# Kernel tuning notes

Hardware: AMD Instinct MI355X
Metric: run time of the kernel (lower is better)

## Reference

```python
import jax, jax.numpy as jnp
import numpy as np

B, T, D, H, L, V = 2, 1024, 1024, 16, 4, 32000
HS = D // H  # head_size = 64


def setup_inputs() -> dict:
    key = jax.random.key(0)
    ks = jax.random.split(key, 15)
    s = 0.02
    return {
        "idx": jax.random.randint(ks[0], (B, T), 0, V, dtype=jnp.int32),
        "tok_emb": jax.random.normal(ks[1], (V, D), jnp.float32) * s,
        "pos_emb": jax.random.normal(ks[2], (T, D), jnp.float32) * s,
        "Wq": jax.random.normal(ks[3], (L, H, D, HS), jnp.float32) * s,
        "Wk": jax.random.normal(ks[4], (L, H, D, HS), jnp.float32) * s,
        "Wv": jax.random.normal(ks[5], (L, H, D, HS), jnp.float32) * s,
        "Wproj": jax.random.normal(ks[6], (L, D, D), jnp.float32) * s,
        "bproj": jnp.zeros((L, D), jnp.float32),
        "W1": jax.random.normal(ks[7], (L, D, 4 * D), jnp.float32) * s,
        "b1": jnp.zeros((L, 4 * D), jnp.float32),
        "W2": jax.random.normal(ks[8], (L, 4 * D, D), jnp.float32) * s,
        "b2": jnp.zeros((L, D), jnp.float32),
        "Wlm": jax.random.normal(ks[9], (D, V), jnp.float32) * s,
        "blm": jnp.zeros((V,), jnp.float32),
    }


def reference(idx, tok_emb, pos_emb, Wq, Wk, Wv, Wproj, bproj, W1, b1, W2, b2, Wlm, blm):
    Bn, Tn = idx.shape
    Dn = tok_emb.shape[1]
    x = tok_emb[idx] + pos_emb[jnp.arange(Tn)][None, :, :]  # (B,T,D)
    causal = jnp.tril(jnp.ones((Tn, Tn), dtype=bool))
    # NOTE: original scales by C**-0.5 where C = embedding_dim (not head_size)
    scale = Dn ** -0.5
    n_layers = Wq.shape[0]
    for l in range(n_layers):
        q = jnp.einsum('btd,hdk->bhtk', x, Wq[l])
        k = jnp.einsum('btd,hdk->bhtk', x, Wk[l])
        v = jnp.einsum('btd,hdk->bhtk', x, Wv[l])
        scores = jnp.einsum('bhtk,bhsk->bhts', q, k) * scale
        scores = jnp.where(causal[None, None, :, :], scores, -jnp.inf)
        probs = jax.nn.softmax(scores, axis=-1)
        attn = jnp.einsum('bhts,bhsk->bhtk', probs, v)
        # concat heads in head order -> (B,T,H*HS)
        attn = attn.transpose(0, 2, 1, 3).reshape(Bn, Tn, Dn)
        x = x + attn @ Wproj[l] + bproj[l]
        h = jax.nn.relu(x @ W1[l] + b1[l])
        x = x + h @ W2[l] + b2[l]
    return x @ Wlm + blm  # (B,T,V) logits
```

## Files before the change

### kernel.cpp

```cpp
#include <hip/hip_runtime.h>
#include <stdint.h>

#define DEVI static __device__ __forceinline__

typedef __attribute__((ext_vector_type(8))) _Float16  f16x8;
typedef __attribute__((ext_vector_type(8))) uint16_t  u16x8;
typedef __attribute__((ext_vector_type(4))) uint16_t  u16x4;
typedef __attribute__((ext_vector_type(4))) float     f32x4;

DEVI uint16_t f2h(float f){ return __builtin_bit_cast(uint16_t, (_Float16)f); }

DEVI void gload_lds16(const void* g, void* l){
  __builtin_amdgcn_global_load_lds((__attribute__((address_space(1))) void*)g,
                                   (__attribute__((address_space(3))) void*)l, 16, 0, 0);
}
DEVI f16x8 frag_ld(const void* base, int byteoff){
  const u16x8* p = (const u16x8*)((const char*)base + byteoff);
  return __builtin_bit_cast(f16x8, *p);
}

__global__ __launch_bounds__(256) void transpose_f32_f16(
    const float* __restrict__ in, uint16_t* __restrict__ out,
    int ld_in, int ld_out,
    long long in_z, long long out_zA, long long out_zB, int zdiv)
{
  __shared__ float tile[64][65];
  const int r0 = blockIdx.x * 64, c0 = blockIdx.y * 64;
  const int z  = blockIdx.z;
  const float* inp = in + (long long)z * in_z;
  uint16_t* outp = out + (long long)(z / zdiv) * out_zA + (long long)(z % zdiv) * out_zB;
  const int r16 = threadIdx.x >> 4, c4 = (threadIdx.x & 15) * 4;
  #pragma unroll
  for (int i = 0; i < 4; i++){
    int r = i * 16 + r16;
    const float4 v = *(const float4*)(inp + (long long)(r0 + r) * ld_in + (c0 + c4));
    tile[r][c4] = v.x; tile[r][c4 + 1] = v.y; tile[r][c4 + 2] = v.z; tile[r][c4 + 3] = v.w;
  }
  __syncthreads();
  const int rp = (threadIdx.x & 31) * 2;
  const int cy = threadIdx.x >> 5;
  #pragma unroll
  for (int i = 0; i < 8; i++){
    int c = i * 8 + cy;
    uint32_t v = (uint32_t)f2h(tile[rp][c]) | ((uint32_t)f2h(tile[rp + 1][c]) << 16);
    *(uint32_t*)(outp + (long long)(c0 + c) * ld_out + (r0 + rp)) = v;
  }
}

__global__ __launch_bounds__(256) void embed_kernel(
    const int* __restrict__ idx, const float* __restrict__ tok,
    const float* __restrict__ pos, float* __restrict__ xf, uint16_t* __restrict__ xb)
{
  const int t = blockIdx.x;
  const int d = threadIdx.x * 4;
  const int token = idx[t];
  const int tp = t & 1023;
  const float4 tv = *(const float4*)(tok + (size_t)token * 1024 + d);
  const float4 pv = *(const float4*)(pos + (size_t)tp * 1024 + d);
  float4 s; s.x = tv.x + pv.x; s.y = tv.y + pv.y; s.z = tv.z + pv.z; s.w = tv.w + pv.w;
  *(float4*)(xf + (size_t)t * 1024 + d) = s;
  uint16_t* o = xb + (size_t)t * 1024 + d;
  o[0] = f2h(s.x); o[1] = f2h(s.y); o[2] = f2h(s.z); o[3] = f2h(s.w);
}

template<bool SPLITK, bool BIAS, bool RELU, bool RES, bool OUTF, bool OUTB, bool QSCALE>
__global__ __launch_bounds__(256, 3) void gemm_bt(
    const uint16_t* __restrict__ A, const uint16_t* __restrict__ Bt,
    const float* __restrict__ bias, const float* __restrict__ res,
    float* __restrict__ outf, uint16_t* __restrict__ outb,
    int M, int N, int K)
{
  __shared__ __align__(16) uint16_t As[128 * 64];
  __shared__ __align__(16) uint16_t Bs[128 * 64];
  const int tid = threadIdx.x, lane = tid & 63, wid = tid >> 6;

  const int Mt = M >> 7;
  int flat = blockIdx.x;
  int kidx = 0;
  if constexpr (SPLITK){ kidx = flat & 1; flat >>= 1; }
  const int total = SPLITK ? (gridDim.x >> 1) : gridDim.x;
  const int wg = (flat & 7) * (total >> 3) + (flat >> 3);
  const int bm = (wg % Mt) * 128, bn = (wg / Mt) * 128;
  int k0 = 0, k1 = K;
  if constexpr (SPLITK){ const int Kh = K >> 1; k0 = kidx * Kh; k1 = k0 + Kh; }
  float* outp = outf;
  if constexpr (SPLITK) outp = outf + (size_t)kidx * M * N;

  const uint16_t* gA[4]; const uint16_t* gB[4];
  #pragma unroll
  for (int i = 0; i < 4; i++){
    int c = i * 256 + tid;
    int row = c >> 3;
    int p = (c * 16) ^ ((row & 7) << 4);
    int off = (p >> 1) & 63;
    gA[i] = A  + (size_t)(bm + row) * K + off;
    gB[i] = Bt + (size_t)(bn + row) * K + off;
  }

  f32x4 acc[4][4];
  const f32x4 fz = {0.f, 0.f, 0.f, 0.f};
  #pragma unroll
  for (int a = 0; a < 4; a++)
    #pragma unroll
    for (int n = 0; n < 4; n++) acc[a][n] = fz;

  const int lrow = lane & 15, lk2 = (lane >> 4) * 16;
  const int wr = (wid >> 1) * 64, wc = (wid & 1) * 64;

  for (int kt = k0; kt < k1; kt += 64){
    #pragma unroll
    for (int i = 0; i < 4; i++)
      gload_lds16(gA[i] + kt, (char*)As + (i * 256 + wid * 64) * 16);
    #pragma unroll
    for (int i = 0; i < 4; i++)
      gload_lds16(gB[i] + kt, (char*)Bs + (i * 256 + wid * 64) * 16);
    __syncthreads();
    #pragma unroll
    for (int kk = 0; kk < 2; kk++){
      f16x8 af[4], bfv[4];
      #pragma unroll
      for (int mf = 0; mf < 4; mf++){
        int row = wr + mf * 16 + lrow;
        af[mf] = frag_ld(As, (row * 128 + kk * 64 + lk2) ^ ((row & 7) << 4));
      }
      #pragma unroll
      for (int nf = 0; nf < 4; nf++){
        int row = wc + nf * 16 + lrow;
        bfv[nf] = frag_ld(Bs, (row * 128 + kk * 64 + lk2) ^ ((row & 7) << 4));
      }
      #pragma unroll
      for (int mf = 0; mf < 4; mf++)
        #pragma unroll
        for (int nf = 0; nf < 4; nf++)
          acc[mf][nf] = __builtin_amdgcn_mfma_f32_16x16x32_f16(af[mf], bfv[nf], acc[mf][nf], 0, 0, 0);
    }
    __syncthreads();
  }

  #pragma unroll
  for (int mf = 0; mf < 4; mf++){
    const int row0 = bm + wr + mf * 16 + (lane >> 4) * 4;
    #pragma unroll
    for (int nf = 0; nf < 4; nf++){
      const int col = bn + wc + nf * 16 + (lane & 15);
      float bv = 0.f;
      if constexpr (BIAS) bv = bias[col];
      float qs = 1.0f;
      if constexpr (QSCALE) qs = (col < 1024) ? 0.03125f : 1.0f;
      #pragma unroll
      for (int j = 0; j < 4; j++){
        float v = acc[mf][nf][j] + bv;
        size_t oi = (size_t)(row0 + j) * N + col;
        if constexpr (RES)  v += res[oi];
        if constexpr (RELU) v = fmaxf(v, 0.f);
        if constexpr (OUTF) outp[oi] = v;
        if constexpr (OUTB) outb[oi] = f2h(v * qs);
      }
    }
  }
}

__global__ __launch_bounds__(256, 2) void gemm_lm(
    const uint16_t* __restrict__ A, const uint16_t* __restrict__ Bt,
    const float* __restrict__ bias, float* __restrict__ outf,
    int M, int N, int K)
{
  __shared__ __align__(16) uint16_t As[128 * 64];
  __shared__ __align__(16) uint16_t Bs[256 * 64];
  const int tid = threadIdx.x, lane = tid & 63, wid = tid >> 6;

  const int Mt = M >> 7;
  const int flat = blockIdx.x;
  const int wg = (flat & 7) * (gridDim.x >> 3) + (flat >> 3);
  const int bm = (wg % Mt) * 128, bn = (wg / Mt) * 256;

  const uint16_t* gA[4]; const uint16_t* gB[8];
  #pragma unroll
  for (int i = 0; i < 4; i++){
    int c = i * 256 + tid;
    int row = c >> 3;
    int p = (c * 16) ^ ((row & 7) << 4);
    int off = (p >> 1) & 63;
    gA[i] = A + (size_t)(bm + row) * K + off;
  }
  #pragma unroll
  for (int i = 0; i < 8; i++){
    int c = i * 256 + tid;
    int row = c >> 3;
    int p = (c * 16) ^ ((row & 7) << 4);
    int off = (p >> 1) & 63;
    gB[i] = Bt + (size_t)(bn + row) * K + off;
  }

  f32x4 acc[4][8];
  const f32x4 fz = {0.f, 0.f, 0.f, 0.f};
  #pragma unroll
  for (int a = 0; a < 4; a++)
    #pragma unroll
    for (int n = 0; n < 8; n++) acc[a][n] = fz;

  const int lrow = lane & 15, lk2 = (lane >> 4) * 16;
  const int wr = (wid >> 1) * 64, wc = (wid & 1) * 128;

  for (int kt = 0; kt < K; kt += 64){
    #pragma unroll
    for (int i = 0; i < 4; i++)
      gload_lds16(gA[i] + kt, (char*)As + (i * 256 + wid * 64) * 16);
    #pragma unroll
    for (int i = 0; i < 8; i++)
      gload_lds16(gB[i] + kt, (char*)Bs + (i * 256 + wid * 64) * 16);
    __syncthreads();
    #pragma unroll
    for (int kk = 0; kk < 2; kk++){
      f16x8 af[4], bfv[8];
      #pragma unroll
      for (int mf = 0; mf < 4; mf++){
        int row = wr + mf * 16 + lrow;
        af[mf] = frag_ld(As, (row * 128 + kk * 64 + lk2) ^ ((row & 7) << 4));
      }
      #pragma unroll
      for (int nf = 0; nf < 8; nf++){
        int row = wc + nf * 16 + lrow;
        bfv[nf] = frag_ld(Bs, (row * 128 + kk * 64 + lk2) ^ ((row & 7) << 4));
      }
      #pragma unroll
      for (int mf = 0; mf < 4; mf++)
        #pragma unroll
        for (int nf = 0; nf < 8; nf++)
          acc[mf][nf] = __builtin_amdgcn_mfma_f32_16x16x32_f16(af[mf], bfv[nf], acc[mf][nf], 0, 0, 0);
    }
    __syncthreads();
  }

  #pragma unroll
  for (int mf = 0; mf < 4; mf++){
    const int row0 = bm + wr + mf * 16 + (lane >> 4) * 4;
    #pragma unroll
    for (int nf = 0; nf < 8; nf++){
      const int col = bn + wc + nf * 16 + (lane & 15);
      const float bv = bias[col];
      #pragma unroll
      for (int j = 0; j < 4; j++)
        outf[(size_t)(row0 + j) * N + col] = acc[mf][nf][j] + bv;
    }
  }
}

__global__ __launch_bounds__(256) void reduce_sk(
    const float* __restrict__ p, const float* __restrict__ bias,
    float* __restrict__ xf, uint16_t* __restrict__ xb, int MN, int N)
{
  const int i = (blockIdx.x * 256 + threadIdx.x) * 4;
  const float4 a = *(const float4*)(p + i);
  const float4 b = *(const float4*)(p + MN + i);
  const int col = i & (N - 1);
  const float4 bv = *(const float4*)(bias + col);
  float4 x = *(float4*)(xf + i);
  x.x += a.x + b.x + bv.x;
  x.y += a.y + b.y + bv.y;
  x.z += a.z + b.z + bv.z;
  x.w += a.w + b.w + bv.w;
  *(float4*)(xf + i) = x;
  uint16_t* o = xb + i;
  o[0] = f2h(x.x); o[1] = f2h(x.y); o[2] = f2h(x.z); o[3] = f2h(x.w);
}

__global__ __launch_bounds__(256, 2) void attn_kernel(
    const uint16_t* __restrict__ qkv, uint16_t* __restrict__ out)
{
  const int bi = blockIdx.x;
  const int b  = bi >> 8;
  const int jj = bi & 255;
  const int h  = jj >> 4;
  int q64 = jj & 15;
  if (b) q64 = 15 - q64;

  __shared__ __align__(16) uint16_t Qs[64 * 64];
  __shared__ __align__(16) uint16_t Ks[128 * 64];
  __shared__ __align__(16) uint16_t Vt[64 * 128];
  __shared__ __align__(16) uint16_t Ps[64 * 128];

  const int tid = threadIdx.x, lane = tid & 63, wid = tid >> 6;
  const size_t bt0 = (size_t)b * 1024;

  int rowC[4], offC[4];
  #pragma unroll
  for (int i = 0; i < 4; i++){
    int c = i * 256 + tid;
    int row = c >> 3;
    int p = (c * 16) ^ ((row & 7) << 4);
    rowC[i] = row; offC[i] = (p >> 1) & 63;
  }

  #pragma unroll
  for (int i = 0; i < 2; i++)
    gload_lds16(qkv + (bt0 + q64 * 64 + rowC[i]) * 3072 + h * 64 + offC[i],
                (char*)Qs + (i * 256 + wid * 64) * 16);
  __syncthreads();

  const int lrow = lane & 15, lk2 = (lane >> 4) * 16, g4 = (lane >> 4) * 4;

  f16x8 aq[2];
  {
    int row = wid * 16 + lrow;
    #pragma unroll
    for (int kk = 0; kk < 2; kk++)
      aq[kk] = frag_ld(Qs, (row * 128 + kk * 64 + lk2) ^ ((row & 7) << 4));
  }

  float l_run[4];
  f32x4 acc_o[4];
  const f32x4 fz = {0.f, 0.f, 0.f, 0.f};
  #pragma unroll
  for (int j = 0; j < 4; j++){ l_run[j] = 0.f; acc_o[j] = fz; }

  const int tpV = (tid >> 3) * 2, d0V = (tid & 7) * 8;
  const int nkt = q64 >> 1;

  for (int kt = 0; kt <= nkt; ++kt){
    __syncthreads();
    #pragma unroll
    for (int i = 0; i < 4; i++)
      gload_lds16(qkv + (bt0 + kt * 128 + rowC[i]) * 3072 + 1024 + h * 64 + offC[i],
                  (char*)Ks + (i * 256 + wid * 64) * 16);
    #pragma unroll
    for (int i = 0; i < 2; i++){
      const int t = i * 64 + tpV;
      const uint16_t* src = qkv + (bt0 + kt * 128 + t) * 3072 + 2048 + h * 64 + d0V;
      const u16x8 v0 = *(const u16x8*)src;
      const u16x8 v1 = *(const u16x8*)(src + 3072);
      #pragma unroll
      for (int dd = 0; dd < 8; dd++){
        const int d = d0V + dd;
        const int byte = (d * 256 + t * 2) ^ ((((d >> 3) ^ d) & 15) << 4);
        *(uint32_t*)((char*)Vt + byte) = (uint32_t)v0[dd] | ((uint32_t)v1[dd] << 16);
      }
    }
    __syncthreads();

    f32x4 sf[8];
    #pragma unroll
    for (int n = 0; n < 8; n++) sf[n] = fz;
    __builtin_amdgcn_s_setprio(1);
    #pragma unroll
    for (int kk = 0; kk < 2; kk++){
      #pragma unroll
      for (int nf = 0; nf < 8; nf++){
        const int row = nf * 16 + lrow;
        const f16x8 bk = frag_ld(Ks, (row * 128 + kk * 64 + lk2) ^ ((row & 7) << 4));
        sf[nf] = __builtin_amdgcn_mfma_f32_16x16x32_f16(aq[kk], bk, sf[nf], 0, 0, 0);
      }
    }
    __builtin_amdgcn_s_setprio(0);

    const bool diag = (kt == nkt);
    #pragma unroll
    for (int j = 0; j < 4; j++){
      float ps = 0.f;
      if (diag){
        const int rg = q64 * 64 + wid * 16 + g4 + j;
        #pragma unroll
        for (int nf = 0; nf < 8; nf++){
          const int cg = kt * 128 + nf * 16 + lrow;
          const float p = (cg <= rg) ? __expf(sf[nf][j]) : 0.f;
          sf[nf][j] = p;
          ps += p;
        }
      } else {
        #pragma unroll
        for (int nf = 0; nf < 8; nf++){
          const float p = __expf(sf[nf][j]);
          sf[nf][j] = p;
          ps += p;
        }
      }
      l_run[j] += ps;
      const int rl = wid * 16 + g4 + j;
      const int sw = (((rl >> 3) ^ rl) & 15) << 4;
      #pragma unroll
      for (int nf = 0; nf < 8; nf++){
        const int byte = (rl * 256 + (nf * 16 + lrow) * 2) ^ sw;
        *(uint16_t*)((char*)Ps + byte) = f2h(sf[nf][j]);
      }
    }
    __syncthreads();

    __builtin_amdgcn_s_setprio(1);
    #pragma unroll
    for (int kk = 0; kk < 4; kk++){
      const int row = wid * 16 + lrow;
      const f16x8 pa = frag_ld(Ps, (row * 256 + kk * 64 + lk2) ^ ((((row >> 3) ^ row) & 15) << 4));
      #pragma unroll
      for (int nh = 0; nh < 4; nh++){
        const int n = nh * 16 + lrow;
        const f16x8 vb = frag_ld(Vt, (n * 256 + kk * 64 + lk2) ^ ((((n >> 3) ^ n) & 15) << 4));
        acc_o[nh] = __builtin_amdgcn_mfma_f32_16x16x32_f16(pa, vb, acc_o[nh], 0, 0, 0);
      }
    }
    __builtin_amdgcn_s_setprio(0);
  }

  #pragma unroll
  for (int j = 0; j < 4; j++){
    #pragma unroll
    for (int mk = 1; mk < 16; mk <<= 1) l_run[j] += __shfl_xor(l_run[j], mk);
  }

  #pragma unroll
  for (int j = 0; j < 4; j++){
    const float inv = 1.f / l_run[j];
    const int rg = q64 * 64 + wid * 16 + g4 + j;
    #pragma unroll
    for (int nh = 0; nh < 4; nh++)
      out[(bt0 + rg) * 1024 + h * 64 + nh * 16 + lrow] = f2h(acc_o[nh][j] * inv);
  }
}

extern "C" void kernel_launch(void* const* d_in, const int* in_sizes, int n_in,
                              void* d_out, int out_size, void* d_ws, size_t ws_size,
                              hipStream_t stream)
{
  const int*   idx   = (const int*)  d_in[0];
  const float* tok   = (const float*)d_in[1];
  const float* pos   = (const float*)d_in[2];
  const float* Wq    = (const float*)d_in[3];
  const float* Wk    = (const float*)d_in[4];
  const float* Wv    = (const float*)d_in[5];
  const float* Wproj = (const float*)d_in[6];
  const float* bproj = (const float*)d_in[7];
  const float* W1    = (const float*)d_in[8];
  const float* b1    = (const float*)d_in[9];
  const float* W2    = (const float*)d_in[10];
  const float* b2    = (const float*)d_in[11];
  const float* Wlm   = (const float*)d_in[12];
  const float* blm   = (const float*)d_in[13];
  float* out = (float*)d_out;

  char* ws = (char*)d_ws;
  size_t off = 0;
  auto alloc = [&](size_t bytes){ void* p = ws + off; off += (bytes + 255) & ~(size_t)255; return p; };
  uint16_t* qkvT   = (uint16_t*)alloc((size_t)4 * 3072 * 1024 * 2);
  uint16_t* WprojT = (uint16_t*)alloc((size_t)4 * 1024 * 1024 * 2);
  uint16_t* W1T    = (uint16_t*)alloc((size_t)4 * 4096 * 1024 * 2);
  uint16_t* W2T    = (uint16_t*)alloc((size_t)4 * 1024 * 4096 * 2);
  uint16_t* WlmT   = (uint16_t*)alloc((size_t)32000 * 1024 * 2);
  float*    xf     = (float*)   alloc((size_t)2048 * 1024 * 4);
  uint16_t* xb     = (uint16_t*)alloc((size_t)2048 * 1024 * 2);
  uint16_t* qkv_a  = (uint16_t*)alloc((size_t)2048 * 3072 * 2);
  uint16_t* attnb  = (uint16_t*)alloc((size_t)2048 * 1024 * 2);
  uint16_t* hb     = (uint16_t*)alloc((size_t)2048 * 4096 * 2);
  float*    psum   = (float*)   alloc((size_t)2 * 2048 * 1024 * 4);
  (void)ws_size; (void)in_sizes; (void)n_in; (void)out_size;

  const dim3 tb(256);
  const int MN = 2048 * 1024;

  transpose_f32_f16<<<dim3(16, 1, 64), tb, 0, stream>>>(Wq, qkvT,                 64, 1024,
      65536LL, 3072LL * 1024, 64LL * 1024, 16);
  transpose_f32_f16<<<dim3(16, 1, 64), tb, 0, stream>>>(Wk, qkvT + 1024 * 1024,   64, 1024,
      65536LL, 3072LL * 1024, 64LL * 1024, 16);
  transpose_f32_f16<<<dim3(16, 1, 64), tb, 0, stream>>>(Wv, qkvT + 2048 * 1024,   64, 1024,
      65536LL, 3072LL * 1024, 64LL * 1024, 16);
  transpose_f32_f16<<<dim3(16, 16, 4), tb, 0, stream>>>(Wproj, WprojT, 1024, 1024,
      1048576LL, 1048576LL, 0LL, 1);
  transpose_f32_f16<<<dim3(16, 64, 4), tb, 0, stream>>>(W1, W1T, 4096, 1024,
      4194304LL, 4194304LL, 0LL, 1);
  transpose_f32_f16<<<dim3(64, 16, 4), tb, 0, stream>>>(W2, W2T, 1024, 4096,
      4194304LL, 4194304LL, 0LL, 1);
  transpose_f32_f16<<<dim3(16, 500, 1), tb, 0, stream>>>(Wlm, WlmT, 32000, 1024,
      0LL, 0LL, 0LL, 1);

  embed_kernel<<<dim3(2048), tb, 0, stream>>>(idx, tok, pos, xf, xb);

  for (int l = 0; l < 4; ++l){
    const uint16_t* qkvT_l = qkvT + (size_t)l * 3072 * 1024;
    gemm_bt<false, false, false, false, false, true, true><<<dim3(384), tb, 0, stream>>>(
        xb, qkvT_l, nullptr, nullptr, nullptr, qkv_a, 2048, 3072, 1024);
    attn_kernel<<<dim3(512), tb, 0, stream>>>(qkv_a, attnb);
    gemm_bt<false, true, false, true, true, true, false><<<dim3(128), tb, 0, stream>>>(
        attnb, WprojT + (size_t)l * 1048576, bproj + l * 1024, xf, xf, xb, 2048, 1024, 1024);
    gemm_bt<false, true, true, false, false, true, false><<<dim3(512), tb, 0, stream>>>(
        xb, W1T + (size_t)l * 4194304, b1 + l * 4096, nullptr, nullptr, hb, 2048, 4096, 1024);
    gemm_bt<true, false, false, false, true, false, false><<<dim3(256), tb, 0, stream>>>(
        hb, W2T + (size_t)l * 4194304, nullptr, nullptr, psum, nullptr, 2048, 1024, 4096);
    reduce_sk<<<dim3(2048), tb, 0, stream>>>(psum, b2 + l * 1024, xf, xb, MN, 1024);
  }

  gemm_lm<<<dim3(2000), tb, 0, stream>>>(xb, WlmT, blm, out, 2048, 32000, 1024);
}
```

Measured before the change: 905.7 us.

## Double-buffer LDS and use 8 waves in LM-head GEMM

Rewrites the LM-head GEMM to run 512 threads (8 waves, each computing a 64x64 subtile) with two LDS buffers. Loads for tile t+2 are issued while tile t is computed, using explicit vmcnt waits, barriers and setprio. The aim is to hide global-to-LDS load latency behind MFMA work. The cost is one block per CU, with double the LDS footprint, and a per-wave fragment reuse ratio lower than the previous 64x128 wave tile.

```diff
diff --git a/kernel.cpp b/kernel.cpp
--- a/kernel.cpp
+++ b/kernel.cpp
@@ -160,13 +160,13 @@
   }
 }
 
-__global__ __launch_bounds__(256, 2) void gemm_lm(
+__global__ __launch_bounds__(512, 1) void gemm_lm(
     const uint16_t* __restrict__ A, const uint16_t* __restrict__ Bt,
     const float* __restrict__ bias, float* __restrict__ outf,
     int M, int N, int K)
 {
-  __shared__ __align__(16) uint16_t As[128 * 64];
-  __shared__ __align__(16) uint16_t Bs[256 * 64];
+  __shared__ __align__(16) uint16_t As[2][128 * 64];
+  __shared__ __align__(16) uint16_t Bs[2][256 * 64];
   const int tid = threadIdx.x, lane = tid & 63, wid = tid >> 6;
 
   const int Mt = M >> 7;
@@ -174,70 +174,97 @@
   const int wg = (flat & 7) * (gridDim.x >> 3) + (flat >> 3);
   const int bm = (wg % Mt) * 128, bn = (wg / Mt) * 256;
 
-  const uint16_t* gA[4]; const uint16_t* gB[8];
-  #pragma unroll
-  for (int i = 0; i < 4; i++){
-    int c = i * 256 + tid;
+  const uint16_t* gA[2]; const uint16_t* gB[4];
+  #pragma unroll
+  for (int i = 0; i < 2; i++){
+    int c = i * 512 + tid;
     int row = c >> 3;
     int p = (c * 16) ^ ((row & 7) << 4);
     int off = (p >> 1) & 63;
     gA[i] = A + (size_t)(bm + row) * K + off;
   }
   #pragma unroll
-  for (int i = 0; i < 8; i++){
-    int c = i * 256 + tid;
+  for (int i = 0; i < 4; i++){
+    int c = i * 512 + tid;
     int row = c >> 3;
     int p = (c * 16) ^ ((row & 7) << 4);
     int off = (p >> 1) & 63;
     gB[i] = Bt + (size_t)(bn + row) * K + off;
   }
 
-  f32x4 acc[4][8];
+  f32x4 acc[4][4];
   const f32x4 fz = {0.f, 0.f, 0.f, 0.f};
   #pragma unroll
   for (int a = 0; a < 4; a++)
     #pragma unroll
-    for (int n = 0; n < 8; n++) acc[a][n] = fz;
+    for (int n = 0; n < 4; n++) acc[a][n] = fz;
 
   const int lrow = lane & 15, lk2 = (lane >> 4) * 16;
-  const int wr = (wid >> 1) * 64, wc = (wid & 1) * 128;
-
-  for (int kt = 0; kt < K; kt += 64){
+  const int wr = (wid >> 2) * 64, wc = (wid & 3) * 64;
+
+  auto stage = [&](int buf, int kt){
+    #pragma unroll
+    for (int i = 0; i < 2; i++)
+      gload_lds16(gA[i] + kt, (char*)As[buf] + (i * 512 + wid * 64) * 16);
     #pragma unroll
     for (int i = 0; i < 4; i++)
-      gload_lds16(gA[i] + kt, (char*)As + (i * 256 + wid * 64) * 16);
-    #pragma unroll
-    for (int i = 0; i < 8; i++)
-      gload_lds16(gB[i] + kt, (char*)Bs + (i * 256 + wid * 64) * 16);
-    __syncthreads();
+      gload_lds16(gB[i] + kt, (char*)Bs[buf] + (i * 512 + wid * 64) * 16);
+  };
+  auto compute = [&](int buf){
     #pragma unroll
     for (int kk = 0; kk < 2; kk++){
-      f16x8 af[4], bfv[8];
+      f16x8 af[4], bfv[4];
       #pragma unroll
       for (int mf = 0; mf < 4; mf++){
         int row = wr + mf * 16 + lrow;
-        af[mf] = frag_ld(As, (row * 128 + kk * 64 + lk2) ^ ((row & 7) << 4));
-      }
-      #pragma unroll
-      for (int nf = 0; nf < 8; nf++){
+        af[mf] = frag_ld(As[buf], (row * 128 + kk * 64 + lk2) ^ ((row & 7) << 4));
+      }
+      #pragma unroll
+      for (int nf = 0; nf < 4; nf++){
         int row = wc + nf * 16 + lrow;
-        bfv[nf] = frag_ld(Bs, (row * 128 + kk * 64 + lk2) ^ ((row & 7) << 4));
+        bfv[nf] = frag_ld(Bs[buf], (row * 128 + kk * 64 + lk2) ^ ((row & 7) << 4));
       }
       #pragma unroll
       for (int mf = 0; mf < 4; mf++)
         #pragma unroll
-        for (int nf = 0; nf < 8; nf++)
+        for (int nf = 0; nf < 4; nf++)
           acc[mf][nf] = __builtin_amdgcn_mfma_f32_16x16x32_f16(af[mf], bfv[nf], acc[mf][nf], 0, 0, 0);
     }
-    __syncthreads();
+  };
+
+  stage(0, 0);
+  stage(1, 64);
+  asm volatile("s_waitcnt vmcnt(6)" ::: "memory");
+  __builtin_amdgcn_sched_barrier(0);
+  __builtin_amdgcn_s_barrier();
+  __builtin_amdgcn_sched_barrier(0);
+
+  const int nt = K >> 6;
+  for (int t = 0; t < nt; ++t){
+    const int cur = t & 1;
+    __builtin_amdgcn_s_setprio(1);
+    compute(cur);
+    __builtin_amdgcn_s_setprio(0);
+    __builtin_amdgcn_sched_barrier(0);
+    __builtin_amdgcn_s_barrier();
+    __builtin_amdgcn_sched_barrier(0);
+    if (t + 2 < nt){
+      stage(cur, (t + 2) * 64);
+      asm volatile("s_waitcnt vmcnt(6)" ::: "memory");
+    } else {
+      asm volatile("s_waitcnt vmcnt(0)" ::: "memory");
+    }
+    __builtin_amdgcn_sched_barrier(0);
+    __builtin_amdgcn_s_barrier();
+    __builtin_amdgcn_sched_barrier(0);
   }
 
   #pragma unroll
   for (int mf = 0; mf < 4; mf++){
     const int row0 = bm + wr + mf * 16 + (lane >> 4) * 4;
     #pragma unroll
-    for (int nf = 0; nf < 8; nf++){
-      const int col = bn + wc + nf * 16 + (lane & 15);
+    for (int nf = 0; nf < 4; nf++){
+      const int col = bn + wc + nf * 16 + lrow;
       const float bv = bias[col];
       #pragma unroll
       for (int j = 0; j < 4; j++)
@@ -486,5 +513,5 @@
     reduce_sk<<<dim3(2048), tb, 0, stream>>>(psum, b2 + l * 1024, xf, xb, MN, 1024);
   }
 
-  gemm_lm<<<dim3(2000), tb, 0, stream>>>(xb, WlmT, blm, out, 2048, 32000, 1024);
-}
+  gemm_lm<<<dim3(2000), dim3(512), 0, stream>>>(xb, WlmT, blm, out, 2048, 32000, 1024);
+}
```

New measurement: 978.0 us. +8.0%, slower.
